# Optimization experiments

Measured on AMD Instinct MI355X. Metric: run time of the kernel, lower is better.

The kernel has to match this reference:

```python
import jax, jax.numpy as jnp
import numpy as np

N = 50000
E = 1600000
NEG_SLOPE = 0.2  # PyG GATConv default
EPS = 1e-16


def gat_conv(x, src, dst, W, att_src, att_dst, bias, concat):
    """One PyG-style GATConv layer. src/dst include self-loops.
    x: (N, in_ch); W: (in_ch, H*C); att_*: (H, C); bias: (H*C,) or (C,).
    """
    H, C = att_src.shape
    h = (x @ W).reshape(N, H, C)                       # per-head features
    a_src = jnp.sum(h * att_src[None], axis=-1)        # (N, H)
    a_dst = jnp.sum(h * att_dst[None], axis=-1)        # (N, H)
    e = jax.nn.leaky_relu(a_src[src] + a_dst[dst], NEG_SLOPE)   # (E', H)
    # segment softmax over incoming edges of each destination node
    m = jax.ops.segment_max(e, dst, num_segments=N)    # (N, H)
    ex = jnp.exp(e - m[dst])
    s = jax.ops.segment_sum(ex, dst, num_segments=N)   # (N, H)
    alpha = ex / (s[dst] + EPS)                        # (E', H)
    out = jax.ops.segment_sum(h[src] * alpha[:, :, None], dst, num_segments=N)  # (N, H, C)
    if concat:
        out = out.reshape(N, H * C)
    else:
        out = out.mean(axis=1)
    return out + bias


def setup_inputs() -> dict:
    key = jax.random.key(0)
    ks = jax.random.split(key, 16)
    g = lambda k, sh: (jax.random.normal(k, sh, jnp.float32) * 0.1)
    return {
        "x": jax.random.normal(ks[0], (N, 64), jnp.float32),
        "edge_index": jax.random.randint(ks[1], (2, E), 0, N, dtype=jnp.int64),
        "batch": jnp.zeros((N,), jnp.int64),
        "W0": g(ks[2], (64, 64)),  "as0": g(ks[3], (8, 8)),  "ad0": g(ks[4], (8, 8)),  "b0": g(ks[5], (64,)),
        "W1": g(ks[6], (64, 64)),  "as1": g(ks[7], (8, 8)),  "ad1": g(ks[8], (8, 8)),  "b1": g(ks[9], (64,)),
        "W2": g(ks[10], (64, 32)), "as2": g(ks[11], (1, 32)), "ad2": g(ks[12], (1, 32)), "b2": g(ks[13], (32,)),
    }


def reference(x, edge_index, batch, W0, as0, ad0, b0, W1, as1, ad1, b1, W2, as2, ad2, b2):
    # add self-loops (PyG GATConv default add_self_loops=True)
    loop = jnp.arange(N, dtype=edge_index.dtype)
    src = jnp.concatenate([edge_index[0], loop])
    dst = jnp.concatenate([edge_index[1], loop])
    h = gat_conv(x, src, dst, W0, as0, ad0, b0, concat=True)
    h = jax.nn.elu(h)  # dropout inactive in eval mode
    h = gat_conv(h, src, dst, W1, as1, ad1, b1, concat=True)
    h = jax.nn.elu(h)
    out = gat_conv(h, src, dst, W2, as2, ad2, b2, concat=False)
    return out
```

## Files before the change

### kernel.cpp

```cpp
#include <hip/hip_runtime.h>
#include <hip/hip_bf16.h>


__device__ __forceinline__ float lrelu(float x) { return x > 0.f ? x : 0.2f * x; }
__device__ __forceinline__ float bflo(unsigned u) { return __uint_as_float(u << 16); }
__device__ __forceinline__ float bfhi(unsigned u) { return __uint_as_float(u & 0xFFFF0000u); }
__device__ __forceinline__ unsigned bfpack(float lo, float hi) {
    __hip_bfloat16 a = __float2bfloat16(lo), b = __float2bfloat16(hi);
    unsigned short ua = *(unsigned short*)&a, ub = *(unsigned short*)&b;
    return (unsigned)ua | ((unsigned)ub << 16);
}

#define PCHUNK 8192
#define CAPB 2688

__global__ __launch_bounds__(256) void partition_direct(const int* __restrict__ edges,
                                                        int E, int n, int NB,
                                                        int* __restrict__ bcursor,
                                                        unsigned* __restrict__ T) {
    __shared__ int hist[1024];
    __shared__ int base[1024];
    int EP = E + n;
    int e0 = blockIdx.x * PCHUNK;
    int e1 = min(EP, e0 + PCHUNK);
    for (int i = threadIdx.x; i < NB; i += 256) hist[i] = 0;
    __syncthreads();
    unsigned cache[32];
#pragma unroll
    for (int k = 0; k < 32; k++) {
        int e = e0 + threadIdx.x + k * 256;
        unsigned v = 0xFFFFFFFFu;
        if (e < e1) {
            int s, d;
            if (e < E) { s = edges[e]; d = edges[E + e]; }
            else       { s = e - E;    d = e - E; }
            unsigned b = (unsigned)d >> 6;
            v = (unsigned)s | ((unsigned)(d & 63) << 16) | (b << 22);
            atomicAdd(&hist[b], 1);
        }
        cache[k] = v;
    }
    __syncthreads();
    for (int i = threadIdx.x; i < NB; i += 256) {
        int c = hist[i];
        base[i] = c ? atomicAdd(&bcursor[i], c) : 0;
        hist[i] = 0;
    }
    __syncthreads();
#pragma unroll
    for (int k = 0; k < 32; k++) {
        unsigned v = cache[k];
        if (v != 0xFFFFFFFFu) {
            unsigned b = v >> 22;
            int r = base[b] + atomicAdd(&hist[b], 1);
            if (r < CAPB) T[(size_t)b * CAPB + r] = v & 0x3FFFFFu;
        }
    }
}

__global__ __launch_bounds__(256) void bucket_sort_direct(const unsigned* __restrict__ T,
                                                          const int* __restrict__ bcursor,
                                                          int n, int* __restrict__ row_ptr,
                                                          int* __restrict__ deg,
                                                          int* __restrict__ ssrc) {
    __shared__ int cnt[64];
    int b = blockIdx.x;
    int total = min(bcursor[b], CAPB);
    int s0 = b * CAPB;
    int node0 = b << 6;
    if (threadIdx.x < 64) cnt[threadIdx.x] = 0;
    __syncthreads();
    for (int i = threadIdx.x; i < total; i += 256)
        atomicAdd(&cnt[(T[s0 + i] >> 16) & 63], 1);
    __syncthreads();
    if (threadIdx.x < 64) {
        int v = cnt[threadIdx.x];
        int p = v;
        for (int o = 1; o < 64; o <<= 1) {
            int t = __shfl_up(p, o);
            if ((int)threadIdx.x >= o) p += t;
        }
        int excl = p - v;
        int node = node0 + threadIdx.x;
        if (node < n) { row_ptr[node] = s0 + excl; deg[node] = v; }
        cnt[threadIdx.x] = excl;
    }
    __syncthreads();
    for (int i = threadIdx.x; i < total; i += 256) {
        unsigned t = T[s0 + i];
        int r = atomicAdd(&cnt[(t >> 16) & 63], 1);
        ssrc[s0 + r] = (int)(t & 0xFFFFu);
    }
}

template <int OUT, int H, typename TIn>
__global__ __launch_bounds__(256) void gemm_att(const TIn* __restrict__ X,
                                                const float* __restrict__ W,
                                                const float* __restrict__ att_s,
                                                const float* __restrict__ att_d,
                                                __hip_bfloat16* __restrict__ Hout,
                                                float* __restrict__ a_src,
                                                float* __restrict__ a_dst, int n) {
    constexpr int C = OUT / H;
    constexpr int CG = OUT / 4;
    constexpr int RPP = 256 / CG;
    constexpr int NPASS = 64 / RPP;
    constexpr int L = C / 4;
    constexpr int PX = 68;
    __shared__ float  xs[64][PX];
    __shared__ float4 ws4[64][CG];
    int tid = threadIdx.x;
    int row0 = blockIdx.x * 64;
    for (int i = tid; i < 64 * CG; i += 256)
        ws4[i / CG][i % CG] = ((const float4*)W)[i];
    if constexpr (sizeof(TIn) == 4) {
        for (int i = tid; i < 64 * 16; i += 256) {
            int r = i / 16, c4 = i % 16;
            int gr = row0 + r;
            float4 v = make_float4(0.f, 0.f, 0.f, 0.f);
            if (gr < n) v = ((const float4*)(X + (size_t)gr * 64))[c4];
            *(float4*)&xs[r][c4 * 4] = v;
        }
    } else {
        for (int i = tid; i < 64 * 8; i += 256) {
            int r = i / 8, g = i % 8;
            int gr = row0 + r;
            uint4 v = make_uint4(0u, 0u, 0u, 0u);
            if (gr < n) v = ((const uint4*)(X + (size_t)gr * 64))[g];
            float* xp = &xs[r][g * 8];
            xp[0] = bflo(v.x); xp[1] = bfhi(v.x);
            xp[2] = bflo(v.y); xp[3] = bfhi(v.y);
            xp[4] = bflo(v.z); xp[5] = bfhi(v.z);
            xp[6] = bflo(v.w); xp[7] = bfhi(v.w);
        }
    }
    __syncthreads();
    const int c4 = tid % CG;
    const int r_in = tid / CG;
    const float4 as4 = ((const float4*)att_s)[c4];
    const float4 ad4 = ((const float4*)att_d)[c4];
#pragma unroll
    for (int pass = 0; pass < NPASS; pass++) {
        int r = r_in + pass * RPP;
        int gr = row0 + r;
        float4 acc = make_float4(0.f, 0.f, 0.f, 0.f);
#pragma unroll
        for (int k = 0; k < 64; k++) {
            float xv = xs[r][k];
            float4 wv = ws4[k][c4];
            acc.x += xv * wv.x; acc.y += xv * wv.y;
            acc.z += xv * wv.z; acc.w += xv * wv.w;
        }
        bool ok = gr < n;
        if (ok) {
            uint2 packed = make_uint2(bfpack(acc.x, acc.y), bfpack(acc.z, acc.w));
            *(uint2*)(Hout + (size_t)gr * OUT + c4 * 4) = packed;
        }
        float ts = acc.x * as4.x + acc.y * as4.y + acc.z * as4.z + acc.w * as4.w;
        float td = acc.x * ad4.x + acc.y * ad4.y + acc.z * ad4.z + acc.w * ad4.w;
#pragma unroll
        for (int m = 1; m < L; m <<= 1) {
            ts += __shfl_xor(ts, m);
            td += __shfl_xor(td, m);
        }
        if (ok && (c4 % L) == 0) {
            int head = (c4 * 4) / C;
            a_src[(size_t)gr * H + head] = ts;
            a_dst[(size_t)gr * H + head] = td;
        }
    }
}

template <int H, int C, bool DO_ELU, typename TOut>
__global__ __launch_bounds__(256) void aggregate(
    const int* __restrict__ row_ptr, const int* __restrict__ deg,
    const int* __restrict__ ssrc,
    const __hip_bfloat16* __restrict__ Hf, const float* __restrict__ a_src,
    const float* __restrict__ a_dst, const float* __restrict__ bias,
    TOut* __restrict__ Xout, int n) {
    constexpr int HC = H * C;
    constexpr int LPR = HC / 8;
    constexpr int EPG = 64 / LPR;
    int wid = (blockIdx.x * blockDim.x + threadIdx.x) >> 6;
    if (wid >= n) return;
    int lane = threadIdx.x & 63;
    int lr = lane % LPR;
    int sub = lane / LPR;
    int head = (lr * 8) / C;
    int start = row_ptr[wid];
    int nloc = deg[wid];
    float adst = a_dst[(size_t)wid * H + head];
    float ssum = 0.f;
    float2 av[4];
#pragma unroll
    for (int k = 0; k < 4; k++) av[k] = make_float2(0.f, 0.f);
#pragma unroll 1
    for (int i = sub; i < nloc; i += 4 * EPG) {
        int i1 = i + EPG, i2 = i + 2 * EPG, i3 = i + 3 * EPG;
        int s0 = ssrc[start + i];
        int s1 = (i1 < nloc) ? ssrc[start + i1] : s0;
        int s2 = (i2 < nloc) ? ssrc[start + i2] : s0;
        int s3 = (i3 < nloc) ? ssrc[start + i3] : s0;
        float e0 = a_src[(size_t)s0 * H + head];
        float e1 = a_src[(size_t)s1 * H + head];
        float e2 = a_src[(size_t)s2 * H + head];
        float e3 = a_src[(size_t)s3 * H + head];
        uint4 f0 = ((const uint4*)(Hf + (size_t)s0 * HC))[lr];
        uint4 f1 = ((const uint4*)(Hf + (size_t)s1 * HC))[lr];
        uint4 f2 = ((const uint4*)(Hf + (size_t)s2 * HC))[lr];
        uint4 f3 = ((const uint4*)(Hf + (size_t)s3 * HC))[lr];
        float p0 = __expf(lrelu(e0 + adst));
        float p1 = (i1 < nloc) ? __expf(lrelu(e1 + adst)) : 0.f;
        float p2 = (i2 < nloc) ? __expf(lrelu(e2 + adst)) : 0.f;
        float p3 = (i3 < nloc) ? __expf(lrelu(e3 + adst)) : 0.f;
        ssum += (p0 + p1) + (p2 + p3);
        av[0].x += p0 * bflo(f0.x) + p1 * bflo(f1.x) + p2 * bflo(f2.x) + p3 * bflo(f3.x);
        av[0].y += p0 * bfhi(f0.x) + p1 * bfhi(f1.x) + p2 * bfhi(f2.x) + p3 * bfhi(f3.x);
        av[1].x += p0 * bflo(f0.y) + p1 * bflo(f1.y) + p2 * bflo(f2.y) + p3 * bflo(f3.y);
        av[1].y += p0 * bfhi(f0.y) + p1 * bfhi(f1.y) + p2 * bfhi(f2.y) + p3 * bfhi(f3.y);
        av[2].x += p0 * bflo(f0.z) + p1 * bflo(f1.z) + p2 * bflo(f2.z) + p3 * bflo(f3.z);
        av[2].y += p0 * bfhi(f0.z) + p1 * bfhi(f1.z) + p2 * bfhi(f2.z) + p3 * bfhi(f3.z);
        av[3].x += p0 * bflo(f0.w) + p1 * bflo(f1.w) + p2 * bflo(f2.w) + p3 * bflo(f3.w);
        av[3].y += p0 * bfhi(f0.w) + p1 * bfhi(f1.w) + p2 * bfhi(f2.w) + p3 * bfhi(f3.w);
    }
#pragma unroll
    for (int mask = LPR; mask < 64; mask <<= 1) {
        ssum += __shfl_xor(ssum, mask);
#pragma unroll
        for (int k = 0; k < 4; k++) {
            av[k].x += __shfl_xor(av[k].x, mask);
            av[k].y += __shfl_xor(av[k].y, mask);
        }
    }
    if (lane < LPR) {
        float inv = 1.f / (ssum + 1e-16f);
        float4 b0 = ((const float4*)bias)[lr * 2];
        float4 b1 = ((const float4*)bias)[lr * 2 + 1];
        float o[8];
        o[0] = av[0].x * inv + b0.x; o[1] = av[0].y * inv + b0.y;
        o[2] = av[1].x * inv + b0.z; o[3] = av[1].y * inv + b0.w;
        o[4] = av[2].x * inv + b1.x; o[5] = av[2].y * inv + b1.y;
        o[6] = av[3].x * inv + b1.z; o[7] = av[3].y * inv + b1.w;
        if (DO_ELU) {
#pragma unroll
            for (int k = 0; k < 8; k++) o[k] = o[k] > 0.f ? o[k] : (__expf(o[k]) - 1.f);
        }
        if constexpr (sizeof(TOut) == 4) {
            float4* outp = (float4*)((float*)Xout + (size_t)wid * HC);
            outp[lr * 2]     = make_float4(o[0], o[1], o[2], o[3]);
            outp[lr * 2 + 1] = make_float4(o[4], o[5], o[6], o[7]);
        } else {
            uint4 pk = make_uint4(bfpack(o[0], o[1]), bfpack(o[2], o[3]),
                                  bfpack(o[4], o[5]), bfpack(o[6], o[7]));
            *(uint4*)((__hip_bfloat16*)Xout + (size_t)wid * HC + lr * 8) = pk;
        }
    }
}

extern "C" void kernel_launch(void* const* d_in, const int* in_sizes, int n_in,
                              void* d_out, int out_size, void* d_ws, size_t ws_size,
                              hipStream_t stream) {
    const float* x     = (const float*)d_in[0];
    const int*   edges = (const int*)d_in[1];
    const float* W0 = (const float*)d_in[3];
    const float* as0 = (const float*)d_in[4];
    const float* ad0 = (const float*)d_in[5];
    const float* b0 = (const float*)d_in[6];
    const float* W1 = (const float*)d_in[7];
    const float* as1 = (const float*)d_in[8];
    const float* ad1 = (const float*)d_in[9];
    const float* b1 = (const float*)d_in[10];
    const float* W2 = (const float*)d_in[11];
    const float* as2 = (const float*)d_in[12];
    const float* ad2 = (const float*)d_in[13];
    const float* b2 = (const float*)d_in[14];

    const int n = in_sizes[0] / 64;
    const int E = in_sizes[1] / 2;
    const int EP = E + n;
    const int NB = (n + 63) >> 6;

    char* p = (char*)d_ws;
    auto alloc = [&](size_t bytes) {
        void* q = (void*)p;
        p += (bytes + 255) & ~(size_t)255;
        return q;
    };
    int* bcursor = (int*)alloc((size_t)NB * 4);
    int* row_ptr = (int*)alloc((size_t)n * 4);
    int* deg     = (int*)alloc((size_t)n * 4);
    int* ssrc    = (int*)alloc((size_t)NB * CAPB * 4);
    size_t hbytes = (size_t)n * 64 * 2;
    size_t tbytes = (size_t)NB * CAPB * 4;
    void*  hraw   = alloc(hbytes > tbytes ? hbytes : tbytes);
    __hip_bfloat16* hbuf = (__hip_bfloat16*)hraw;
    unsigned*       T    = (unsigned*)hraw;
    float* a_s = (float*)alloc((size_t)n * 8 * 4);
    float* a_d = (float*)alloc((size_t)n * 8 * 4);
    __hip_bfloat16* feat = (__hip_bfloat16*)alloc((size_t)n * 64 * 2);
    (void)ws_size;

    hipMemsetAsync(bcursor, 0, (size_t)NB * 4, stream);
    partition_direct<<<(EP + PCHUNK - 1) / PCHUNK, 256, 0, stream>>>(edges, E, n, NB,
                                                                     bcursor, T);
    bucket_sort_direct<<<NB, 256, 0, stream>>>(T, bcursor, n, row_ptr, deg, ssrc);

    int gb = (n + 63) / 64;
    int ab = (n + 3) / 4;

    gemm_att<64, 8, float><<<gb, 256, 0, stream>>>(x, W0, as0, ad0, hbuf, a_s, a_d, n);
    aggregate<8, 8, true, __hip_bfloat16><<<ab, 256, 0, stream>>>(
        row_ptr, deg, ssrc, hbuf, a_s, a_d, b0, feat, n);

    gemm_att<64, 8, __hip_bfloat16><<<gb, 256, 0, stream>>>(feat, W1, as1, ad1, hbuf,
                                                            a_s, a_d, n);
    aggregate<8, 8, true, __hip_bfloat16><<<ab, 256, 0, stream>>>(
        row_ptr, deg, ssrc, hbuf, a_s, a_d, b1, feat, n);

    gemm_att<32, 1, __hip_bfloat16><<<gb, 256, 0, stream>>>(feat, W2, as2, ad2, hbuf,
                                                            a_s, a_d, n);
    aggregate<1, 32, false, float><<<ab, 256, 0, stream>>>(
        row_ptr, deg, ssrc, hbuf, a_s, a_d, b2, (float*)d_out, n);
}
```

Before: 196.9 us.

## Fuse aggregation of layers 0/1 with next layer's GEMM and shrink source indices

Layer aggregation is fused with the following layer's projection GEMM. Each 1024-thread block aggregates 64 destination nodes into shared memory (after ELU) and then multiplies by the next weight matrix, so the intermediate bf16 feature tensor no longer goes through global memory and two launches are removed. Sorted source indices are stored as 16-bit values, halving index traffic. The cost is ping-pong buffers for features and attention logits, and larger blocks that may lower occupancy for the latency-bound gather.

```diff
diff --git a/kernel.cpp b/kernel.cpp
--- a/kernel.cpp
+++ b/kernel.cpp
@@ -62,7 +62,7 @@
                                                           const int* __restrict__ bcursor,
                                                           int n, int* __restrict__ row_ptr,
                                                           int* __restrict__ deg,
-                                                          int* __restrict__ ssrc) {
+                                                          unsigned short* __restrict__ ssrc) {
     __shared__ int cnt[64];
     int b = blockIdx.x;
     int total = min(bcursor[b], CAPB);
@@ -89,12 +89,12 @@
     for (int i = threadIdx.x; i < total; i += 256) {
         unsigned t = T[s0 + i];
         int r = atomicAdd(&cnt[(t >> 16) & 63], 1);
-        ssrc[s0 + r] = (int)(t & 0xFFFFu);
-    }
-}
-
-template <int OUT, int H, typename TIn>
-__global__ __launch_bounds__(256) void gemm_att(const TIn* __restrict__ X,
+        ssrc[s0 + r] = (unsigned short)(t & 0xFFFFu);
+    }
+}
+
+template <int OUT, int H>
+__global__ __launch_bounds__(256) void gemm_att(const float* __restrict__ X,
                                                 const float* __restrict__ W,
                                                 const float* __restrict__ att_s,
                                                 const float* __restrict__ att_d,
@@ -113,26 +113,12 @@
     int row0 = blockIdx.x * 64;
     for (int i = tid; i < 64 * CG; i += 256)
         ws4[i / CG][i % CG] = ((const float4*)W)[i];
-    if constexpr (sizeof(TIn) == 4) {
-        for (int i = tid; i < 64 * 16; i += 256) {
-            int r = i / 16, c4 = i % 16;
-            int gr = row0 + r;
-            float4 v = make_float4(0.f, 0.f, 0.f, 0.f);
-            if (gr < n) v = ((const float4*)(X + (size_t)gr * 64))[c4];
-            *(float4*)&xs[r][c4 * 4] = v;
-        }
-    } else {
-        for (int i = tid; i < 64 * 8; i += 256) {
-            int r = i / 8, g = i % 8;
-            int gr = row0 + r;
-            uint4 v = make_uint4(0u, 0u, 0u, 0u);
-            if (gr < n) v = ((const uint4*)(X + (size_t)gr * 64))[g];
-            float* xp = &xs[r][g * 8];
-            xp[0] = bflo(v.x); xp[1] = bfhi(v.x);
-            xp[2] = bflo(v.y); xp[3] = bfhi(v.y);
-            xp[4] = bflo(v.z); xp[5] = bfhi(v.z);
-            xp[6] = bflo(v.w); xp[7] = bfhi(v.w);
-        }
+    for (int i = tid; i < 64 * 16; i += 256) {
+        int r = i / 16, c4 = i % 16;
+        int gr = row0 + r;
+        float4 v = make_float4(0.f, 0.f, 0.f, 0.f);
+        if (gr < n) v = ((const float4*)(X + (size_t)gr * 64))[c4];
+        *(float4*)&xs[r][c4 * 4] = v;
     }
     __syncthreads();
     const int c4 = tid % CG;
@@ -171,13 +157,150 @@
     }
 }
 
-template <int H, int C, bool DO_ELU, typename TOut>
-__global__ __launch_bounds__(256) void aggregate(
+template <int GOUT, int GH>
+__global__ __launch_bounds__(1024) void agg_gemm(
     const int* __restrict__ row_ptr, const int* __restrict__ deg,
-    const int* __restrict__ ssrc,
+    const unsigned short* __restrict__ ssrc,
+    const __hip_bfloat16* __restrict__ Hf, const float* __restrict__ a_srcL,
+    const float* __restrict__ a_dstL, const float* __restrict__ biasL,
+    const float* __restrict__ W, const float* __restrict__ att_s,
+    const float* __restrict__ att_d, __hip_bfloat16* __restrict__ Hout,
+    float* __restrict__ a_src_o, float* __restrict__ a_dst_o, int n) {
+    constexpr int AH = 8;
+    constexpr int LPR = 8;
+    constexpr int EPG = 8;
+    constexpr int GC = GOUT / GH;
+    constexpr int CG = GOUT / 4;
+    constexpr int L = GC / 4;
+    constexpr int PX = 68;
+    __shared__ float  xs[64][PX];
+    __shared__ float4 ws4[64][CG];
+    int tid = threadIdx.x;
+    int row0 = blockIdx.x * 64;
+    for (int i = tid; i < 64 * CG; i += 1024)
+        ws4[i / CG][i % CG] = ((const float4*)W)[i];
+
+    int wv = tid >> 6, lane = tid & 63;
+    int lr = lane % LPR, sub = lane / LPR;
+    int head = lr;
+    for (int it = 0; it < 4; ++it) {
+        int local = wv * 4 + it;
+        int wid = row0 + local;
+        bool live = wid < n;
+        int start = 0, nloc = 0;
+        float adst = 0.f;
+        if (live) {
+            start = row_ptr[wid];
+            nloc = deg[wid];
+            adst = a_dstL[(size_t)wid * AH + head];
+        }
+        float ssum = 0.f;
+        float2 av[4];
+#pragma unroll
+        for (int k = 0; k < 4; k++) av[k] = make_float2(0.f, 0.f);
+#pragma unroll 1
+        for (int i = sub; i < nloc; i += 4 * EPG) {
+            int i1 = i + EPG, i2 = i + 2 * EPG, i3 = i + 3 * EPG;
+            int s0 = ssrc[start + i];
+            int s1 = (i1 < nloc) ? ssrc[start + i1] : s0;
+            int s2 = (i2 < nloc) ? ssrc[start + i2] : s0;
+            int s3 = (i3 < nloc) ? ssrc[start + i3] : s0;
+            float e0 = a_srcL[(size_t)s0 * AH + head];
+            float e1 = a_srcL[(size_t)s1 * AH + head];
+            float e2 = a_srcL[(size_t)s2 * AH + head];
+            float e3 = a_srcL[(size_t)s3 * AH + head];
+            uint4 f0 = ((const uint4*)(Hf + (size_t)s0 * 64))[lr];
+            uint4 f1 = ((const uint4*)(Hf + (size_t)s1 * 64))[lr];
+            uint4 f2 = ((const uint4*)(Hf + (size_t)s2 * 64))[lr];
+            uint4 f3 = ((const uint4*)(Hf + (size_t)s3 * 64))[lr];
+            float p0 = __expf(lrelu(e0 + adst));
+            float p1 = (i1 < nloc) ? __expf(lrelu(e1 + adst)) : 0.f;
+            float p2 = (i2 < nloc) ? __expf(lrelu(e2 + adst)) : 0.f;
+            float p3 = (i3 < nloc) ? __expf(lrelu(e3 + adst)) : 0.f;
+            ssum += (p0 + p1) + (p2 + p3);
+            av[0].x += p0 * bflo(f0.x) + p1 * bflo(f1.x) + p2 * bflo(f2.x) + p3 * bflo(f3.x);
+            av[0].y += p0 * bfhi(f0.x) + p1 * bfhi(f1.x) + p2 * bfhi(f2.x) + p3 * bfhi(f3.x);
+            av[1].x += p0 * bflo(f0.y) + p1 * bflo(f1.y) + p2 * bflo(f2.y) + p3 * bflo(f3.y);
+            av[1].y += p0 * bfhi(f0.y) + p1 * bfhi(f1.y) + p2 * bfhi(f2.y) + p3 * bfhi(f3.y);
+            av[2].x += p0 * bflo(f0.z) + p1 * bflo(f1.z) + p2 * bflo(f2.z) + p3 * bflo(f3.z);
+            av[2].y += p0 * bfhi(f0.z) + p1 * bfhi(f1.z) + p2 * bfhi(f2.z) + p3 * bfhi(f3.z);
+            av[3].x += p0 * bflo(f0.w) + p1 * bflo(f1.w) + p2 * bflo(f2.w) + p3 * bflo(f3.w);
+            av[3].y += p0 * bfhi(f0.w) + p1 * bfhi(f1.w) + p2 * bfhi(f2.w) + p3 * bfhi(f3.w);
+        }
+#pragma unroll
+        for (int mask = LPR; mask < 64; mask <<= 1) {
+            ssum += __shfl_xor(ssum, mask);
+#pragma unroll
+            for (int k = 0; k < 4; k++) {
+                av[k].x += __shfl_xor(av[k].x, mask);
+                av[k].y += __shfl_xor(av[k].y, mask);
+            }
+        }
+        if (lane < LPR) {
+            float o[8];
+            if (live) {
+                float inv = 1.f / (ssum + 1e-16f);
+                float4 b0 = ((const float4*)biasL)[lr * 2];
+                float4 b1 = ((const float4*)biasL)[lr * 2 + 1];
+                o[0] = av[0].x * inv + b0.x; o[1] = av[0].y * inv + b0.y;
+                o[2] = av[1].x * inv + b0.z; o[3] = av[1].y * inv + b0.w;
+                o[4] = av[2].x * inv + b1.x; o[5] = av[2].y * inv + b1.y;
+                o[6] = av[3].x * inv + b1.z; o[7] = av[3].y * inv + b1.w;
+#pragma unroll
+                for (int k = 0; k < 8; k++)
+                    o[k] = o[k] > 0.f ? o[k] : (__expf(o[k]) - 1.f);
+            } else {
+#pragma unroll
+                for (int k = 0; k < 8; k++) o[k] = 0.f;
+            }
+            float* xp = &xs[local][lr * 8];
+#pragma unroll
+            for (int k = 0; k < 8; k++) xp[k] = o[k];
+        }
+    }
+    __syncthreads();
+
+    const int c4 = tid % CG;
+    const int r = tid / CG;
+    if (r < 64) {
+        int gr = row0 + r;
+        float4 acc = make_float4(0.f, 0.f, 0.f, 0.f);
+#pragma unroll
+        for (int k = 0; k < 64; k++) {
+            float xv = xs[r][k];
+            float4 wv4 = ws4[k][c4];
+            acc.x += xv * wv4.x; acc.y += xv * wv4.y;
+            acc.z += xv * wv4.z; acc.w += xv * wv4.w;
+        }
+        bool ok = gr < n;
+        if (ok) {
+            uint2 packed = make_uint2(bfpack(acc.x, acc.y), bfpack(acc.z, acc.w));
+            *(uint2*)(Hout + (size_t)gr * GOUT + c4 * 4) = packed;
+        }
+        const float4 as4 = ((const float4*)att_s)[c4];
+        const float4 ad4 = ((const float4*)att_d)[c4];
+        float ts = acc.x * as4.x + acc.y * as4.y + acc.z * as4.z + acc.w * as4.w;
+        float td = acc.x * ad4.x + acc.y * ad4.y + acc.z * ad4.z + acc.w * ad4.w;
+#pragma unroll
+        for (int m = 1; m < L; m <<= 1) {
+            ts += __shfl_xor(ts, m);
+            td += __shfl_xor(td, m);
+        }
+        if (ok && (c4 % L) == 0) {
+            int h = (c4 * 4) / GC;
+            a_src_o[(size_t)gr * GH + h] = ts;
+            a_dst_o[(size_t)gr * GH + h] = td;
+        }
+    }
+}
+
+template <int H, int C>
+__global__ __launch_bounds__(256) void aggregate_final(
+    const int* __restrict__ row_ptr, const int* __restrict__ deg,
+    const unsigned short* __restrict__ ssrc,
     const __hip_bfloat16* __restrict__ Hf, const float* __restrict__ a_src,
     const float* __restrict__ a_dst, const float* __restrict__ bias,
-    TOut* __restrict__ Xout, int n) {
+    float* __restrict__ Xout, int n) {
     constexpr int HC = H * C;
     constexpr int LPR = HC / 8;
     constexpr int EPG = 64 / LPR;
@@ -236,24 +359,11 @@
         float inv = 1.f / (ssum + 1e-16f);
         float4 b0 = ((const float4*)bias)[lr * 2];
         float4 b1 = ((const float4*)bias)[lr * 2 + 1];
-        float o[8];
-        o[0] = av[0].x * inv + b0.x; o[1] = av[0].y * inv + b0.y;
-        o[2] = av[1].x * inv + b0.z; o[3] = av[1].y * inv + b0.w;
-        o[4] = av[2].x * inv + b1.x; o[5] = av[2].y * inv + b1.y;
-        o[6] = av[3].x * inv + b1.z; o[7] = av[3].y * inv + b1.w;
-        if (DO_ELU) {
-#pragma unroll
-            for (int k = 0; k < 8; k++) o[k] = o[k] > 0.f ? o[k] : (__expf(o[k]) - 1.f);
-        }
-        if constexpr (sizeof(TOut) == 4) {
-            float4* outp = (float4*)((float*)Xout + (size_t)wid * HC);
-            outp[lr * 2]     = make_float4(o[0], o[1], o[2], o[3]);
-            outp[lr * 2 + 1] = make_float4(o[4], o[5], o[6], o[7]);
-        } else {
-            uint4 pk = make_uint4(bfpack(o[0], o[1]), bfpack(o[2], o[3]),
-                                  bfpack(o[4], o[5]), bfpack(o[6], o[7]));
-            *(uint4*)((__hip_bfloat16*)Xout + (size_t)wid * HC + lr * 8) = pk;
-        }
+        float4* outp = (float4*)(Xout + (size_t)wid * HC);
+        outp[lr * 2]     = make_float4(av[0].x * inv + b0.x, av[0].y * inv + b0.y,
+                                       av[1].x * inv + b0.z, av[1].y * inv + b0.w);
+        outp[lr * 2 + 1] = make_float4(av[2].x * inv + b1.x, av[2].y * inv + b1.y,
+                                       av[3].x * inv + b1.z, av[3].y * inv + b1.w);
     }
 }
 
@@ -289,15 +399,17 @@
     int* bcursor = (int*)alloc((size_t)NB * 4);
     int* row_ptr = (int*)alloc((size_t)n * 4);
     int* deg     = (int*)alloc((size_t)n * 4);
-    int* ssrc    = (int*)alloc((size_t)NB * CAPB * 4);
+    unsigned short* ssrc = (unsigned short*)alloc((size_t)NB * CAPB * 2);
     size_t hbytes = (size_t)n * 64 * 2;
     size_t tbytes = (size_t)NB * CAPB * 4;
     void*  hraw   = alloc(hbytes > tbytes ? hbytes : tbytes);
-    __hip_bfloat16* hbuf = (__hip_bfloat16*)hraw;
-    unsigned*       T    = (unsigned*)hraw;
-    float* a_s = (float*)alloc((size_t)n * 8 * 4);
-    float* a_d = (float*)alloc((size_t)n * 8 * 4);
-    __hip_bfloat16* feat = (__hip_bfloat16*)alloc((size_t)n * 64 * 2);
+    __hip_bfloat16* hbufA = (__hip_bfloat16*)hraw;
+    unsigned*       T     = (unsigned*)hraw;
+    __hip_bfloat16* hbufB = (__hip_bfloat16*)alloc((size_t)n * 64 * 2);
+    float* a_s  = (float*)alloc((size_t)n * 8 * 4);
+    float* a_d  = (float*)alloc((size_t)n * 8 * 4);
+    float* a_s2 = (float*)alloc((size_t)n * 8 * 4);
+    float* a_d2 = (float*)alloc((size_t)n * 8 * 4);
     (void)ws_size;
 
     hipMemsetAsync(bcursor, 0, (size_t)NB * 4, stream);
@@ -308,17 +420,14 @@
     int gb = (n + 63) / 64;
     int ab = (n + 3) / 4;
 
-    gemm_att<64, 8, float><<<gb, 256, 0, stream>>>(x, W0, as0, ad0, hbuf, a_s, a_d, n);
-    aggregate<8, 8, true, __hip_bfloat16><<<ab, 256, 0, stream>>>(
-        row_ptr, deg, ssrc, hbuf, a_s, a_d, b0, feat, n);
-
-    gemm_att<64, 8, __hip_bfloat16><<<gb, 256, 0, stream>>>(feat, W1, as1, ad1, hbuf,
-                                                            a_s, a_d, n);
-    aggregate<8, 8, true, __hip_bfloat16><<<ab, 256, 0, stream>>>(
-        row_ptr, deg, ssrc, hbuf, a_s, a_d, b1, feat, n);
-
-    gemm_att<32, 1, __hip_bfloat16><<<gb, 256, 0, stream>>>(feat, W2, as2, ad2, hbuf,
-                                                            a_s, a_d, n);
-    aggregate<1, 32, false, float><<<ab, 256, 0, stream>>>(
-        row_ptr, deg, ssrc, hbuf, a_s, a_d, b2, (float*)d_out, n);
-}
+    gemm_att<64, 8><<<gb, 256, 0, stream>>>(x, W0, as0, ad0, hbufA, a_s, a_d, n);
+
+    agg_gemm<64, 8><<<gb, 1024, 0, stream>>>(row_ptr, deg, ssrc, hbufA, a_s, a_d, b0,
+                                             W1, as1, ad1, hbufB, a_s2, a_d2, n);
+
+    agg_gemm<32, 1><<<gb, 1024, 0, stream>>>(row_ptr, deg, ssrc, hbufB, a_s2, a_d2, b1,
+                                             W2, as2, ad2, hbufA, a_s, a_d, n);
+
+    aggregate_final<1, 32><<<ab, 256, 0, stream>>>(row_ptr, deg, ssrc, hbufA, a_s, a_d,
+                                                   b2, (float*)d_out, n);
+}
```

After: 190.6 us. 1.03x faster.
